# Kernel tuning notes

Hardware: AMD Instinct MI355X
Metric: run time of the kernel (lower is better)

## Reference

```python
import jax, jax.numpy as jnp
import numpy as np

K = 3
STRIDE = 1
PAD = 1
DIL = 1


def setup_inputs() -> dict:
    key = jax.random.key(0)
    k1, k2, k3, k4 = jax.random.split(key, 4)
    B, C, H, W = 8, 64, 96, 96
    O = 64
    x = jax.random.normal(k1, (B, C, H, W), jnp.float32)
    # offset-predicting conv is conventionally near-zero init -> small offsets
    w_off = jax.random.normal(k2, (2 * K * K, C, K, K), jnp.float32) * 0.01
    b_off = jax.random.normal(k3, (2 * K * K,), jnp.float32) * 0.01
    w_dcn = jax.random.normal(k4, (O, C, K, K), jnp.float32) * (1.0 / np.sqrt(C * K * K))
    return {"x": x, "w_off": w_off, "b_off": b_off, "w_dcn": w_dcn}


def _deform_conv(x, offset, w_dcn):
    B, C, H, W = x.shape
    O = w_dcn.shape[0]
    Ho, Wo = offset.shape[2], offset.shape[3]
    K2 = K * K
    # torchvision layout: offset[:, 2*k] = dy, offset[:, 2*k+1] = dx, k = ky*K + kx
    off = offset.reshape(B, K2, 2, Ho, Wo)
    kk = jnp.arange(K2)
    ky = (kk // K).astype(jnp.float32)
    kx = (kk % K).astype(jnp.float32)
    base_h = (jnp.arange(Ho) * STRIDE - PAD).astype(jnp.float32)
    base_w = (jnp.arange(Wo) * STRIDE - PAD).astype(jnp.float32)
    # sampling positions, shape [B, K2, Ho, Wo]
    py = off[:, :, 0] + base_h[None, None, :, None] + (ky * DIL)[None, :, None, None]
    px = off[:, :, 1] + base_w[None, None, None, :] + (kx * DIL)[None, :, None, None]

    y0 = jnp.floor(py)
    x0 = jnp.floor(px)
    wy = py - y0
    wx = px - x0
    y0i = y0.astype(jnp.int32)
    x0i = x0.astype(jnp.int32)
    y1i = y0i + 1
    x1i = x0i + 1

    x_flat = x.reshape(B, C, H * W)
    N = K2 * Ho * Wo

    def gather(yi, xi):
        valid = (yi >= 0) & (yi < H) & (xi >= 0) & (xi < W)
        lin = jnp.clip(yi, 0, H - 1) * W + jnp.clip(xi, 0, W - 1)  # [B,K2,Ho,Wo]
        idx = jnp.broadcast_to(lin.reshape(B, 1, N), (B, C, N))
        v = jnp.take_along_axis(x_flat, idx, axis=2).reshape(B, C, K2, Ho, Wo)
        return v * valid[:, None].astype(x.dtype)

    w00 = ((1 - wy) * (1 - wx))[:, None]
    w01 = ((1 - wy) * wx)[:, None]
    w10 = (wy * (1 - wx))[:, None]
    w11 = (wy * wx)[:, None]
    sampled = (gather(y0i, x0i) * w00 + gather(y0i, x1i) * w01
               + gather(y1i, x0i) * w10 + gather(y1i, x1i) * w11)  # [B,C,K2,Ho,Wo]

    # deformable conv = contraction over (c_in, kernel pos); bias=False
    return jnp.einsum('bckhw,ock->bohw', sampled, w_dcn.reshape(O, C, K2))


def reference(x, w_off, b_off, w_dcn):
    offset = jax.lax.conv_general_dilated(
        x, w_off, window_strides=(STRIDE, STRIDE), padding=[(PAD, PAD), (PAD, PAD)],
        rhs_dilation=(DIL, DIL), dimension_numbers=('NCHW', 'OIHW', 'NCHW'))
    offset = offset + b_off[None, :, None, None]
    return _deform_conv(x, offset, w_dcn)
```

## Files before the change

kernel.cpp:

```cpp
#include <hip/hip_runtime.h>

#define BB 8
#define CC 64
#define HH 96
#define WW 96
#define OO 64
#define KK 3
#define K2 9
#define HW (HH*WW)
#define NOFF 18
#define NPIX (BB*HW)
#define MT 64
#define NTILE (HW/MT)
#define NXCD 8
#define WR 6
#define WC 36
#define NWIN (WR*WC)
#define OSTR 21

typedef _Float16 f16;
typedef __attribute__((ext_vector_type(2))) _Float16 f16x2;
typedef __attribute__((ext_vector_type(4))) _Float16 f16x4;
typedef __attribute__((ext_vector_type(4))) float f32x4;
typedef __attribute__((ext_vector_type(2))) unsigned int uint2v;
typedef __attribute__((ext_vector_type(4))) unsigned int uint4v;

#define MFMA16(a,b,c) __builtin_amdgcn_mfma_f32_16x16x16f16(a,b,c,0,0,0)

__device__ __forceinline__ f16x2 bch(unsigned u) { return __builtin_bit_cast(f16x2, u); }
__device__ __forceinline__ unsigned bcu(f16x2 h) { return __builtin_bit_cast(unsigned, h); }
__device__ __forceinline__ f16x4 fq(unsigned a, unsigned b) {
  uint2v u = {a, b};
  return __builtin_bit_cast(f16x4, u);
}
__device__ __forceinline__ f16x4 fq2(uint2v u) { return __builtin_bit_cast(f16x4, u); }
__device__ __forceinline__ int xcd_remap(int bid, int per) {
  return (bid & 7) * per + (bid >> 3);
}

__global__ __launch_bounds__(256) void transpose_kernel(
    const float* __restrict__ x, unsigned short* __restrict__ xt) {
  int t = threadIdx.x;
  int px = xcd_remap(blockIdx.x, NPIX / 64 / NXCD) * 64 + (t & 63);
  int cg = t >> 6;
  int b = px / HW, hw = px % HW;
  const float* xp = x + (size_t)b * CC * HW + (size_t)(cg * 16) * HW + hw;
  f16 r[16];
  #pragma unroll
  for (int i = 0; i < 16; ++i) r[i] = (f16)xp[i * HW];
  uint4v v0, v1;
  #pragma unroll
  for (int q = 0; q < 4; ++q) {
    f16x2 a = {r[q*2], r[q*2+1]};       v0[q] = bcu(a);
    f16x2 bq = {r[8+q*2], r[8+q*2+1]};  v1[q] = bcu(bq);
  }
  uint4v* dst = (uint4v*)(xt + (size_t)px * CC + cg * 16);
  dst[0] = v0; dst[1] = v1;
}

__global__ void wprep_kernel(const float* __restrict__ w_dcn,
                             unsigned short* __restrict__ wtx) {
  int idx = blockIdx.x * 256 + threadIdx.x;
  int e = idx & 15;
  int l = (idx >> 4) & 63;
  int nb = (idx >> 10) & 3;
  int k = idx >> 12;
  int c = 16 * (l >> 4) + e;
  int o = nb * 16 + (l & 15);
  f16 h = (f16)w_dcn[(o * CC + c) * K2 + k];
  wtx[idx] = __builtin_bit_cast(unsigned short, h);
}

__global__ void woffprep_kernel(const float* __restrict__ w_off,
                                unsigned short* __restrict__ wofx) {
  int idx = blockIdx.x * 256 + threadIdx.x;
  int e = idx & 3;
  int l = (idx >> 2) & 63;
  int q = (idx >> 8) & 3;
  int n = (idx >> 10) & 1;
  int kt = idx >> 11;
  int c = q * 16 + 4 * (l >> 4) + e;
  int j = n * 16 + (l & 15);
  f16 h = (f16)((j < NOFF) ? w_off[(j * CC + c) * K2 + kt] : 0.f);
  wofx[idx] = __builtin_bit_cast(unsigned short, h);
}

#define XWIN_OFF 0
#define OFFS_OFF 27648
#define ACCX_OFF 0
#define SMEM_SZ  33024

__global__ __launch_bounds__(512, 4) void fused_kernel(
    const unsigned short* __restrict__ xt,
    const unsigned short* __restrict__ wofx,
    const float* __restrict__ b_off,
    const unsigned short* __restrict__ wtx,
    float* __restrict__ out) {
  __shared__ __align__(16) char smem[SMEM_SZ];
  char* xwin = smem + XWIN_OFF;
  float* offs = (float*)(smem + OFFS_OFF);
  float* accx = (float*)(smem + ACCX_OFF);

  int t = threadIdx.x;
  int blk = xcd_remap(blockIdx.x, NPIX / MT / NXCD);
  int b = blk / NTILE;
  int ti = blk % NTILE;
  int tr = ti / 3, tc = ti % 3;
  int h0 = tr * 2, w0 = tc * 32;
  int hw0 = h0 * WW + w0;

  const char* xb = (const char*)(xt + (size_t)b * HW * CC);

  #pragma unroll
  for (int r = 0; r < 4; ++r) {
    int d = r * 512 + t;
    if (d < NWIN * 8) {
      int row = d >> 3, sg = d & 7;
      int wr_ = row / WC, wc_ = row - wr_ * WC;
      int gy = h0 - 2 + wr_;
      int gx = w0 - 2 + wc_;
      uint4v v = (uint4v){0u, 0u, 0u, 0u};
      if (((unsigned)gy < HH) && ((unsigned)gx < WW))
        v = *(const uint4v*)(xb + (size_t)((gy * WW + gx) << 7) + (sg << 4));
      *(uint4v*)&xwin[row * 128 + ((sg ^ (row & 7)) << 4)] = v;
    }
  }
  __syncthreads();

  int wv = t >> 6;
  int l  = t & 63;
  int lr = l & 15, lh = l >> 4;

  {
    int m = wv & 3, n = wv >> 2;
    int p = m * 16 + lr;
    int prow = ((p >> 5) + 1) * WC + (p & 31) + 1;
    f32x4 accO = (f32x4){0.f, 0.f, 0.f, 0.f};
    #pragma unroll
    for (int kt = 0; kt < K2; ++kt) {
      int wrow = prow + (kt / 3) * WC + (kt % 3);
      int rs = wrow & 7;
      const char* bp = (const char*)wofx + (((size_t)(kt * 2 + n) * 4) * 64 + l) * 8;
      #pragma unroll
      for (int q = 0; q < 4; ++q) {
        uint2v a2 = *(const uint2v*)&xwin[wrow * 128
                      + ((((q << 1) + (lh >> 1)) ^ rs) << 4) + ((lh & 1) << 3)];
        uint2v b2 = *(const uint2v*)(bp + (size_t)q * (64 * 8));
        accO = MFMA16(fq2(a2), fq2(b2), accO);
      }
    }
    int j = n * 16 + lr;
    if (j < NOFF) {
      float bj = b_off[j];
      #pragma unroll
      for (int r = 0; r < 4; ++r) {
        int px = m * 16 + lh * 4 + r;
        offs[px * OSTR + j] = accO[r] + bj;
      }
    }
  }
  __syncthreads();

  int grp = wv >> 2;
  int base = grp * 5;
  int cnt  = 5 - grp;
  int Ra = (wv & 3) * 16 + lr;
  int hpix = h0 + (Ra >> 5), wpix = w0 + (Ra & 31);
  int cB = lh * 32;

  unsigned po01[5], po23[5], pw01[5], pw23[5];
  unsigned emask = 0;
  #pragma unroll
  for (int i = 0; i < 5; ++i) {
    po01[i] = 0; po23[i] = 0; pw01[i] = 0; pw23[i] = 0;
    if (i < cnt) {
      int kt = base + i;
      int ky = kt / 3, kx = kt % 3;
      float py = offs[Ra * OSTR + 2 * kt]     + (float)(hpix - 1 + ky);
      float px = offs[Ra * OSTR + 2 * kt + 1] + (float)(wpix - 1 + kx);
      float y0f = floorf(py), x0f = floorf(px);
      float wy = py - y0f, wx = px - x0f;
      int y0 = (int)y0f, x0 = (int)x0f;
      int y1 = y0 + 1, x1 = x0 + 1;
      bool vy0 = (unsigned)y0 < HH, vy1 = (unsigned)y1 < HH;
      bool vx0 = (unsigned)x0 < WW, vx1 = (unsigned)x1 < WW;
      int cy0 = min(max(y0, 0), HH - 1), cy1 = min(max(y1, 0), HH - 1);
      int cx0 = min(max(x0, 0), WW - 1), cx1 = min(max(x1, 0), WW - 1);
      float g00 = (1.f - wy) * (1.f - wx) * ((vy0 && vx0) ? 1.f : 0.f);
      float g01 = (1.f - wy) * wx         * ((vy0 && vx1) ? 1.f : 0.f);
      float g10 = wy * (1.f - wx)         * ((vy1 && vx0) ? 1.f : 0.f);
      float g11 = wy * wx                 * ((vy1 && vx1) ? 1.f : 0.f);
      int ry0 = cy0 - (h0 - 2), ry1 = cy1 - (h0 - 2);
      int rx0 = cx0 - (w0 - 2), rx1 = cx1 - (w0 - 2);
      bool inw = ((unsigned)ry0 < WR) && ((unsigned)ry1 < WR) &&
                 ((unsigned)rx0 < WC) && ((unsigned)rx1 < WC);
      if (inw) {
        po01[i] = (unsigned)((ry0 * WC + rx0) << 7)
                | ((unsigned)((ry0 * WC + rx1) << 7) << 16);
        po23[i] = (unsigned)((ry1 * WC + rx0) << 7)
                | ((unsigned)((ry1 * WC + rx1) << 7) << 16);
      } else {
        po01[i] = (unsigned)(cy0 * WW + cx0)
                | ((unsigned)(cy0 * WW + cx1) << 16) | 0x80000000u;
        po23[i] = (unsigned)(cy1 * WW + cx0)
                | ((unsigned)(cy1 * WW + cx1) << 16);
        emask |= 1u << i;
      }
      f16x2 wa = {(f16)g00, (f16)g01};
      f16x2 wb = {(f16)g10, (f16)g11};
      pw01[i] = bcu(wa);
      pw23[i] = bcu(wb);
    }
  }

  f32x4 acc[4];
  #pragma unroll
  for (int nb = 0; nb < 4; ++nb) acc[nb] = (f32x4){0.f, 0.f, 0.f, 0.f};

  #define WREAD(bo, pos) (*(const uint4v*)&xwin[(bo) + ((pos) << 4)])
  if (__ballot(emask != 0) == 0ull) {
    #pragma unroll
    for (int i = 0; i < 5; ++i) {
      if (i < cnt) {
        unsigned e0 = po01[i], e1 = po23[i];
        int i0 = (int)(e0 & 0xffffu), i1 = (int)(e0 >> 16);
        int i2 = (int)(e1 & 0xffffu), i3 = (int)(e1 >> 16);
        int s0 = lh * 2;
        uint4v c0a = WREAD(i0, s0 ^ ((i0 >> 7) & 7));
        uint4v c0b = WREAD(i0, (s0 + 1) ^ ((i0 >> 7) & 7));
        uint4v c1a = WREAD(i1, s0 ^ ((i1 >> 7) & 7));
        uint4v c1b = WREAD(i1, (s0 + 1) ^ ((i1 >> 7) & 7));
        uint4v c2a = WREAD(i2, s0 ^ ((i2 >> 7) & 7));
        uint4v c2b = WREAD(i2, (s0 + 1) ^ ((i2 >> 7) & 7));
        uint4v c3a = WREAD(i3, s0 ^ ((i3 >> 7) & 7));
        uint4v c3b = WREAD(i3, (s0 + 1) ^ ((i3 >> 7) & 7));
        f16x2 wA = bch(pw01[i]), wB = bch(pw23[i]);
        f16x2 p0 = {wA[0], wA[0]}, p1 = {wA[1], wA[1]};
        f16x2 p2 = {wB[0], wB[0]}, p3 = {wB[1], wB[1]};
        uint4v pa, pb2;
        #pragma unroll
        for (int q = 0; q < 4; ++q) {
          f16x2 s  = p0 * bch(c0a[q]) + p1 * bch(c1a[q])
                   + p2 * bch(c2a[q]) + p3 * bch(c3a[q]);
          pa[q] = bcu(s);
          f16x2 s2 = p0 * bch(c0b[q]) + p1 * bch(c1b[q])
                   + p2 * bch(c2b[q]) + p3 * bch(c3b[q]);
          pb2[q] = bcu(s2);
        }
        f16x4 a0 = fq(pa[0],  pa[1]);
        f16x4 a1 = fq(pa[2],  pa[3]);
        f16x4 a2 = fq(pb2[0], pb2[1]);
        f16x4 a3 = fq(pb2[2], pb2[3]);
        const char* wbase = (const char*)wtx
                          + (((size_t)(base + i) * 4) * 64 + l) * 32;
        #pragma unroll
        for (int nb = 0; nb < 4; ++nb) {
          const char* wp = wbase + (size_t)nb * (64 * 32);
          uint4v u0 = *(const uint4v*)wp;
          uint4v u1 = *(const uint4v*)(wp + 16);
          acc[nb] = MFMA16(a0, fq(u0[0], u0[1]), acc[nb]);
          acc[nb] = MFMA16(a1, fq(u0[2], u0[3]), acc[nb]);
          acc[nb] = MFMA16(a2, fq(u1[0], u1[1]), acc[nb]);
          acc[nb] = MFMA16(a3, fq(u1[2], u1[3]), acc[nb]);
        }
      }
    }
  } else {
    #pragma unroll
    for (int i = 0; i < 5; ++i) {
      if (i < cnt) {
        unsigned e0 = po01[i], e1 = po23[i];
        uint4v c0a, c0b, c1a, c1b, c2a, c2b, c3a, c3b;
        if ((int)e0 >= 0) {
          int i0 = (int)(e0 & 0xffffu), i1 = (int)(e0 >> 16);
          int i2 = (int)(e1 & 0xffffu), i3 = (int)(e1 >> 16);
          int s0 = lh * 2;
          c0a = WREAD(i0, s0 ^ ((i0 >> 7) & 7));
          c0b = WREAD(i0, (s0 + 1) ^ ((i0 >> 7) & 7));
          c1a = WREAD(i1, s0 ^ ((i1 >> 7) & 7));
          c1b = WREAD(i1, (s0 + 1) ^ ((i1 >> 7) & 7));
          c2a = WREAD(i2, s0 ^ ((i2 >> 7) & 7));
          c2b = WREAD(i2, (s0 + 1) ^ ((i2 >> 7) & 7));
          c3a = WREAD(i3, s0 ^ ((i3 >> 7) & 7));
          c3b = WREAD(i3, (s0 + 1) ^ ((i3 >> 7) & 7));
        } else {
          int i0 = (int)(e0 & 0x7fffu) << 7;
          int i1 = (int)((e0 >> 16) & 0x7fffu) << 7;
          int i2 = (int)(e1 & 0x7fffu) << 7;
          int i3 = (int)((e1 >> 16) & 0x7fffu) << 7;
          c0a = *(const uint4v*)(xb + i0 + cB);
          c0b = *(const uint4v*)(xb + i0 + cB + 16);
          c1a = *(const uint4v*)(xb + i1 + cB);
          c1b = *(const uint4v*)(xb + i1 + cB + 16);
          c2a = *(const uint4v*)(xb + i2 + cB);
          c2b = *(const uint4v*)(xb + i2 + cB + 16);
          c3a = *(const uint4v*)(xb + i3 + cB);
          c3b = *(const uint4v*)(xb + i3 + cB + 16);
        }
        f16x2 wA = bch(pw01[i]), wB = bch(pw23[i]);
        f16x2 p0 = {wA[0], wA[0]}, p1 = {wA[1], wA[1]};
        f16x2 p2 = {wB[0], wB[0]}, p3 = {wB[1], wB[1]};
        uint4v pa, pb2;
        #pragma unroll
        for (int q = 0; q < 4; ++q) {
          f16x2 s  = p0 * bch(c0a[q]) + p1 * bch(c1a[q])
                   + p2 * bch(c2a[q]) + p3 * bch(c3a[q]);
          pa[q] = bcu(s);
          f16x2 s2 = p0 * bch(c0b[q]) + p1 * bch(c1b[q])
                   + p2 * bch(c2b[q]) + p3 * bch(c3b[q]);
          pb2[q] = bcu(s2);
        }
        f16x4 a0 = fq(pa[0],  pa[1]);
        f16x4 a1 = fq(pa[2],  pa[3]);
        f16x4 a2 = fq(pb2[0], pb2[1]);
        f16x4 a3 = fq(pb2[2], pb2[3]);
        const char* wbase = (const char*)wtx
                          + (((size_t)(base + i) * 4) * 64 + l) * 32;
        #pragma unroll
        for (int nb = 0; nb < 4; ++nb) {
          const char* wp = wbase + (size_t)nb * (64 * 32);
          uint4v u0 = *(const uint4v*)wp;
          uint4v u1 = *(const uint4v*)(wp + 16);
          acc[nb] = MFMA16(a0, fq(u0[0], u0[1]), acc[nb]);
          acc[nb] = MFMA16(a1, fq(u0[2], u0[3]), acc[nb]);
          acc[nb] = MFMA16(a2, fq(u1[0], u1[1]), acc[nb]);
          acc[nb] = MFMA16(a3, fq(u1[2], u1[3]), acc[nb]);
        }
      }
    }
  }
  __syncthreads();

  if (grp == 1) {
    #pragma unroll
    for (int nb = 0; nb < 4; ++nb)
      *(f32x4*)&accx[(nb * 16 + lr) * 68 + (wv & 3) * 16 + lh * 4] = acc[nb];
  }
  __syncthreads();
  if (grp == 0) {
    float* ob = out + (size_t)b * OO * HW;
    #pragma unroll
    for (int nb = 0; nb < 4; ++nb) {
      f32x4 other = *(const f32x4*)&accx[(nb * 16 + lr) * 68 + (wv & 3) * 16 + lh * 4];
      f32x4 v = acc[nb] + other;
      int o = nb * 16 + lr;
      int m = (wv & 3) * 16 + lh * 4;
      int base2 = hw0 + (m >> 5) * WW + (m & 31);
      *(f32x4*)(ob + (size_t)o * HW + base2) = v;
    }
  }
}

extern "C" void kernel_launch(void* const* d_in, const int* in_sizes, int n_in,
                              void* d_out, int out_size, void* d_ws, size_t ws_size,
                              hipStream_t stream) {
  const float* x     = (const float*)d_in[0];
  const float* w_off = (const float*)d_in[1];
  const float* b_off = (const float*)d_in[2];
  const float* w_dcn = (const float*)d_in[3];
  float* out = (float*)d_out;

  char* ws = (char*)d_ws;
  unsigned short* xtp  = (unsigned short*)ws;
  unsigned short* wtx  = (unsigned short*)(ws + 9437184);
  unsigned short* wofx = (unsigned short*)(ws + 9437184 + 73728);

  transpose_kernel<<<NPIX / 64, 256, 0, stream>>>(x, xtp);
  wprep_kernel<<<(K2 * 4 * 64 * 16) / 256, 256, 0, stream>>>(w_dcn, wtx);
  woffprep_kernel<<<(K2 * 2 * 4 * 64 * 4) / 256, 256, 0, stream>>>(w_off, wofx);
  fused_kernel<<<NPIX / MT, 512, 0, stream>>>(xtp, wofx, b_off, wtx, out);
}
```

Before: 47.04 us.

## Double pixel tile per block, drop split-K reduction, merge weight prep kernels

```diff
diff --git a/kernel.cpp b/kernel.cpp
--- a/kernel.cpp
+++ b/kernel.cpp
@@ -10,10 +10,10 @@
 #define HW (HH*WW)
 #define NOFF 18
 #define NPIX (BB*HW)
-#define MT 64
+#define MT 128
 #define NTILE (HW/MT)
 #define NXCD 8
-#define WR 6
+#define WR 8
 #define WC 36
 #define NWIN (WR*WC)
 #define OSTR 21
@@ -58,39 +58,39 @@
   dst[0] = v0; dst[1] = v1;
 }
 
-__global__ void wprep_kernel(const float* __restrict__ w_dcn,
-                             unsigned short* __restrict__ wtx) {
+__global__ void prep_kernel(const float* __restrict__ w_dcn,
+                            const float* __restrict__ w_off,
+                            unsigned short* __restrict__ wtx,
+                            unsigned short* __restrict__ wofx) {
   int idx = blockIdx.x * 256 + threadIdx.x;
-  int e = idx & 15;
-  int l = (idx >> 4) & 63;
-  int nb = (idx >> 10) & 3;
-  int k = idx >> 12;
-  int c = 16 * (l >> 4) + e;
-  int o = nb * 16 + (l & 15);
-  f16 h = (f16)w_dcn[(o * CC + c) * K2 + k];
-  wtx[idx] = __builtin_bit_cast(unsigned short, h);
-}
-
-__global__ void woffprep_kernel(const float* __restrict__ w_off,
-                                unsigned short* __restrict__ wofx) {
-  int idx = blockIdx.x * 256 + threadIdx.x;
-  int e = idx & 3;
-  int l = (idx >> 2) & 63;
-  int q = (idx >> 8) & 3;
-  int n = (idx >> 10) & 1;
-  int kt = idx >> 11;
-  int c = q * 16 + 4 * (l >> 4) + e;
-  int j = n * 16 + (l & 15);
-  f16 h = (f16)((j < NOFF) ? w_off[(j * CC + c) * K2 + kt] : 0.f);
-  wofx[idx] = __builtin_bit_cast(unsigned short, h);
+  if (idx < 36864) {
+    int e = idx & 15;
+    int l = (idx >> 4) & 63;
+    int nb = (idx >> 10) & 3;
+    int k = idx >> 12;
+    int c = 16 * (l >> 4) + e;
+    int o = nb * 16 + (l & 15);
+    f16 h = (f16)w_dcn[(o * CC + c) * K2 + k];
+    wtx[idx] = __builtin_bit_cast(unsigned short, h);
+  } else {
+    int i2 = idx - 36864;
+    int e = i2 & 3;
+    int l = (i2 >> 2) & 63;
+    int q = (i2 >> 8) & 3;
+    int n = (i2 >> 10) & 1;
+    int kt = i2 >> 11;
+    int c = q * 16 + 4 * (l >> 4) + e;
+    int j = n * 16 + (l & 15);
+    f16 h = (f16)((j < NOFF) ? w_off[(j * CC + c) * K2 + kt] : 0.f);
+    wofx[i2] = __builtin_bit_cast(unsigned short, h);
+  }
 }
 
 #define XWIN_OFF 0
-#define OFFS_OFF 27648
-#define ACCX_OFF 0
-#define SMEM_SZ  33024
-
-__global__ __launch_bounds__(512, 4) void fused_kernel(
+#define OFFS_OFF 36864
+#define SMEM_SZ  47616
+
+__global__ __launch_bounds__(512, 3) void fused_kernel(
     const unsigned short* __restrict__ xt,
     const unsigned short* __restrict__ wofx,
     const float* __restrict__ b_off,
@@ -99,20 +99,19 @@
   __shared__ __align__(16) char smem[SMEM_SZ];
   char* xwin = smem + XWIN_OFF;
   float* offs = (float*)(smem + OFFS_OFF);
-  float* accx = (float*)(smem + ACCX_OFF);
 
   int t = threadIdx.x;
   int blk = xcd_remap(blockIdx.x, NPIX / MT / NXCD);
   int b = blk / NTILE;
   int ti = blk % NTILE;
   int tr = ti / 3, tc = ti % 3;
-  int h0 = tr * 2, w0 = tc * 32;
+  int h0 = tr * 4, w0 = tc * 32;
   int hw0 = h0 * WW + w0;
 
   const char* xb = (const char*)(xt + (size_t)b * HW * CC);
 
   #pragma unroll
-  for (int r = 0; r < 4; ++r) {
+  for (int r = 0; r < 5; ++r) {
     int d = r * 512 + t;
     if (d < NWIN * 8) {
       int row = d >> 3, sg = d & 7;
@@ -132,222 +131,210 @@
   int lr = l & 15, lh = l >> 4;
 
   {
-    int m = wv & 3, n = wv >> 2;
-    int p = m * 16 + lr;
+    int p = wv * 16 + lr;
     int prow = ((p >> 5) + 1) * WC + (p & 31) + 1;
-    f32x4 accO = (f32x4){0.f, 0.f, 0.f, 0.f};
+    f32x4 accO0 = (f32x4){0.f, 0.f, 0.f, 0.f};
+    f32x4 accO1 = (f32x4){0.f, 0.f, 0.f, 0.f};
     #pragma unroll
     for (int kt = 0; kt < K2; ++kt) {
       int wrow = prow + (kt / 3) * WC + (kt % 3);
       int rs = wrow & 7;
-      const char* bp = (const char*)wofx + (((size_t)(kt * 2 + n) * 4) * 64 + l) * 8;
+      const char* bp0 = (const char*)wofx + (((size_t)(kt * 2 + 0) * 4) * 64 + l) * 8;
+      const char* bp1 = (const char*)wofx + (((size_t)(kt * 2 + 1) * 4) * 64 + l) * 8;
       #pragma unroll
       for (int q = 0; q < 4; ++q) {
         uint2v a2 = *(const uint2v*)&xwin[wrow * 128
                       + ((((q << 1) + (lh >> 1)) ^ rs) << 4) + ((lh & 1) << 3)];
-        uint2v b2 = *(const uint2v*)(bp + (size_t)q * (64 * 8));
-        accO = MFMA16(fq2(a2), fq2(b2), accO);
-      }
-    }
-    int j = n * 16 + lr;
-    if (j < NOFF) {
+        uint2v b0 = *(const uint2v*)(bp0 + (size_t)q * (64 * 8));
+        uint2v b1 = *(const uint2v*)(bp1 + (size_t)q * (64 * 8));
+        accO0 = MFMA16(fq2(a2), fq2(b0), accO0);
+        accO1 = MFMA16(fq2(a2), fq2(b1), accO1);
+      }
+    }
+    {
+      int j = lr;
       float bj = b_off[j];
       #pragma unroll
       for (int r = 0; r < 4; ++r) {
-        int px = m * 16 + lh * 4 + r;
-        offs[px * OSTR + j] = accO[r] + bj;
+        int px = wv * 16 + lh * 4 + r;
+        offs[px * OSTR + j] = accO0[r] + bj;
+      }
+    }
+    if (lr < 2) {
+      int j = 16 + lr;
+      float bj = b_off[j];
+      #pragma unroll
+      for (int r = 0; r < 4; ++r) {
+        int px = wv * 16 + lh * 4 + r;
+        offs[px * OSTR + j] = accO1[r] + bj;
       }
     }
   }
   __syncthreads();
 
-  int grp = wv >> 2;
-  int base = grp * 5;
-  int cnt  = 5 - grp;
-  int Ra = (wv & 3) * 16 + lr;
+  int Ra = wv * 16 + lr;
   int hpix = h0 + (Ra >> 5), wpix = w0 + (Ra & 31);
   int cB = lh * 32;
 
-  unsigned po01[5], po23[5], pw01[5], pw23[5];
+  unsigned po01[K2], po23[K2], pw01[K2], pw23[K2];
   unsigned emask = 0;
   #pragma unroll
-  for (int i = 0; i < 5; ++i) {
-    po01[i] = 0; po23[i] = 0; pw01[i] = 0; pw23[i] = 0;
-    if (i < cnt) {
-      int kt = base + i;
-      int ky = kt / 3, kx = kt % 3;
-      float py = offs[Ra * OSTR + 2 * kt]     + (float)(hpix - 1 + ky);
-      float px = offs[Ra * OSTR + 2 * kt + 1] + (float)(wpix - 1 + kx);
-      float y0f = floorf(py), x0f = floorf(px);
-      float wy = py - y0f, wx = px - x0f;
-      int y0 = (int)y0f, x0 = (int)x0f;
-      int y1 = y0 + 1, x1 = x0 + 1;
-      bool vy0 = (unsigned)y0 < HH, vy1 = (unsigned)y1 < HH;
-      bool vx0 = (unsigned)x0 < WW, vx1 = (unsigned)x1 < WW;
-      int cy0 = min(max(y0, 0), HH - 1), cy1 = min(max(y1, 0), HH - 1);
-      int cx0 = min(max(x0, 0), WW - 1), cx1 = min(max(x1, 0), WW - 1);
-      float g00 = (1.f - wy) * (1.f - wx) * ((vy0 && vx0) ? 1.f : 0.f);
-      float g01 = (1.f - wy) * wx         * ((vy0 && vx1) ? 1.f : 0.f);
-      float g10 = wy * (1.f - wx)         * ((vy1 && vx0) ? 1.f : 0.f);
-      float g11 = wy * wx                 * ((vy1 && vx1) ? 1.f : 0.f);
-      int ry0 = cy0 - (h0 - 2), ry1 = cy1 - (h0 - 2);
-      int rx0 = cx0 - (w0 - 2), rx1 = cx1 - (w0 - 2);
-      bool inw = ((unsigned)ry0 < WR) && ((unsigned)ry1 < WR) &&
-                 ((unsigned)rx0 < WC) && ((unsigned)rx1 < WC);
-      if (inw) {
-        po01[i] = (unsigned)((ry0 * WC + rx0) << 7)
-                | ((unsigned)((ry0 * WC + rx1) << 7) << 16);
-        po23[i] = (unsigned)((ry1 * WC + rx0) << 7)
-                | ((unsigned)((ry1 * WC + rx1) << 7) << 16);
-      } else {
-        po01[i] = (unsigned)(cy0 * WW + cx0)
-                | ((unsigned)(cy0 * WW + cx1) << 16) | 0x80000000u;
-        po23[i] = (unsigned)(cy1 * WW + cx0)
-                | ((unsigned)(cy1 * WW + cx1) << 16);
-        emask |= 1u << i;
-      }
-      f16x2 wa = {(f16)g00, (f16)g01};
-      f16x2 wb = {(f16)g10, (f16)g11};
-      pw01[i] = bcu(wa);
-      pw23[i] = bcu(wb);
-    }
+  for (int k = 0; k < K2; ++k) {
+    int ky = k / KK, kx = k % KK;
+    float py = offs[Ra * OSTR + 2 * k]     + (float)(hpix - 1 + ky);
+    float px = offs[Ra * OSTR + 2 * k + 1] + (float)(wpix - 1 + kx);
+    float y0f = floorf(py), x0f = floorf(px);
+    float wy = py - y0f, wx = px - x0f;
+    int y0 = (int)y0f, x0 = (int)x0f;
+    int y1 = y0 + 1, x1 = x0 + 1;
+    bool vy0 = (unsigned)y0 < HH, vy1 = (unsigned)y1 < HH;
+    bool vx0 = (unsigned)x0 < WW, vx1 = (unsigned)x1 < WW;
+    int cy0 = min(max(y0, 0), HH - 1), cy1 = min(max(y1, 0), HH - 1);
+    int cx0 = min(max(x0, 0), WW - 1), cx1 = min(max(x1, 0), WW - 1);
+    float g00 = (1.f - wy) * (1.f - wx) * ((vy0 && vx0) ? 1.f : 0.f);
+    float g01 = (1.f - wy) * wx         * ((vy0 && vx1) ? 1.f : 0.f);
+    float g10 = wy * (1.f - wx)         * ((vy1 && vx0) ? 1.f : 0.f);
+    float g11 = wy * wx                 * ((vy1 && vx1) ? 1.f : 0.f);
+    int ry0 = cy0 - (h0 - 2), ry1 = cy1 - (h0 - 2);
+    int rx0 = cx0 - (w0 - 2), rx1 = cx1 - (w0 - 2);
+    bool inw = ((unsigned)ry0 < WR) && ((unsigned)ry1 < WR) &&
+               ((unsigned)rx0 < WC) && ((unsigned)rx1 < WC);
+    if (inw) {
+      po01[k] = (unsigned)(ry0 * WC + rx0)
+              | ((unsigned)(ry0 * WC + rx1) << 16);
+      po23[k] = (unsigned)(ry1 * WC + rx0)
+              | ((unsigned)(ry1 * WC + rx1) << 16);
+    } else {
+      po01[k] = (unsigned)(cy0 * WW + cx0)
+              | ((unsigned)(cy0 * WW + cx1) << 16) | 0x80000000u;
+      po23[k] = (unsigned)(cy1 * WW + cx0)
+              | ((unsigned)(cy1 * WW + cx1) << 16);
+      emask |= 1u << k;
+    }
+    f16x2 wa = {(f16)g00, (f16)g01};
+    f16x2 wb = {(f16)g10, (f16)g11};
+    pw01[k] = bcu(wa);
+    pw23[k] = bcu(wb);
   }
 
   f32x4 acc[4];
   #pragma unroll
   for (int nb = 0; nb < 4; ++nb) acc[nb] = (f32x4){0.f, 0.f, 0.f, 0.f};
 
-  #define WREAD(bo, pos) (*(const uint4v*)&xwin[(bo) + ((pos) << 4)])
+  #define WREAD(ro, pos) (*(const uint4v*)&xwin[((ro) << 7) + ((pos) << 4)])
   if (__ballot(emask != 0) == 0ull) {
     #pragma unroll
-    for (int i = 0; i < 5; ++i) {
-      if (i < cnt) {
-        unsigned e0 = po01[i], e1 = po23[i];
-        int i0 = (int)(e0 & 0xffffu), i1 = (int)(e0 >> 16);
-        int i2 = (int)(e1 & 0xffffu), i3 = (int)(e1 >> 16);
-        int s0 = lh * 2;
-        uint4v c0a = WREAD(i0, s0 ^ ((i0 >> 7) & 7));
-        uint4v c0b = WREAD(i0, (s0 + 1) ^ ((i0 >> 7) & 7));
-        uint4v c1a = WREAD(i1, s0 ^ ((i1 >> 7) & 7));
-        uint4v c1b = WREAD(i1, (s0 + 1) ^ ((i1 >> 7) & 7));
-        uint4v c2a = WREAD(i2, s0 ^ ((i2 >> 7) & 7));
-        uint4v c2b = WREAD(i2, (s0 + 1) ^ ((i2 >> 7) & 7));
-        uint4v c3a = WREAD(i3, s0 ^ ((i3 >> 7) & 7));
-        uint4v c3b = WREAD(i3, (s0 + 1) ^ ((i3 >> 7) & 7));
-        f16x2 wA = bch(pw01[i]), wB = bch(pw23[i]);
-        f16x2 p0 = {wA[0], wA[0]}, p1 = {wA[1], wA[1]};
-        f16x2 p2 = {wB[0], wB[0]}, p3 = {wB[1], wB[1]};
-        uint4v pa, pb2;
-        #pragma unroll
-        for (int q = 0; q < 4; ++q) {
-          f16x2 s  = p0 * bch(c0a[q]) + p1 * bch(c1a[q])
-                   + p2 * bch(c2a[q]) + p3 * bch(c3a[q]);
-          pa[q] = bcu(s);
-          f16x2 s2 = p0 * bch(c0b[q]) + p1 * bch(c1b[q])
-                   + p2 * bch(c2b[q]) + p3 * bch(c3b[q]);
-          pb2[q] = bcu(s2);
-        }
-        f16x4 a0 = fq(pa[0],  pa[1]);
-        f16x4 a1 = fq(pa[2],  pa[3]);
-        f16x4 a2 = fq(pb2[0], pb2[1]);
-        f16x4 a3 = fq(pb2[2], pb2[3]);
-        const char* wbase = (const char*)wtx
-                          + (((size_t)(base + i) * 4) * 64 + l) * 32;
-        #pragma unroll
-        for (int nb = 0; nb < 4; ++nb) {
-          const char* wp = wbase + (size_t)nb * (64 * 32);
-          uint4v u0 = *(const uint4v*)wp;
-          uint4v u1 = *(const uint4v*)(wp + 16);
-          acc[nb] = MFMA16(a0, fq(u0[0], u0[1]), acc[nb]);
-          acc[nb] = MFMA16(a1, fq(u0[2], u0[3]), acc[nb]);
-          acc[nb] = MFMA16(a2, fq(u1[0], u1[1]), acc[nb]);
-          acc[nb] = MFMA16(a3, fq(u1[2], u1[3]), acc[nb]);
-        }
+    for (int k = 0; k < K2; ++k) {
+      unsigned e0 = po01[k], e1 = po23[k];
+      int r0 = (int)(e0 & 0x7fffu), r1 = (int)(e0 >> 16);
+      int r2 = (int)(e1 & 0x7fffu), r3 = (int)(e1 >> 16);
+      int s0 = lh * 2;
+      uint4v c0a = WREAD(r0, s0 ^ (r0 & 7));
+      uint4v c0b = WREAD(r0, (s0 + 1) ^ (r0 & 7));
+      uint4v c1a = WREAD(r1, s0 ^ (r1 & 7));
+      uint4v c1b = WREAD(r1, (s0 + 1) ^ (r1 & 7));
+      uint4v c2a = WREAD(r2, s0 ^ (r2 & 7));
+      uint4v c2b = WREAD(r2, (s0 + 1) ^ (r2 & 7));
+      uint4v c3a = WREAD(r3, s0 ^ (r3 & 7));
+      uint4v c3b = WREAD(r3, (s0 + 1) ^ (r3 & 7));
+      f16x2 wA = bch(pw01[k]), wB = bch(pw23[k]);
+      f16x2 p0 = {wA[0], wA[0]}, p1 = {wA[1], wA[1]};
+      f16x2 p2 = {wB[0], wB[0]}, p3 = {wB[1], wB[1]};
+      uint4v pa, pb2;
+      #pragma unroll
+      for (int q = 0; q < 4; ++q) {
+        f16x2 s  = p0 * bch(c0a[q]) + p1 * bch(c1a[q])
+                 + p2 * bch(c2a[q]) + p3 * bch(c3a[q]);
+        pa[q] = bcu(s);
+        f16x2 s2 = p0 * bch(c0b[q]) + p1 * bch(c1b[q])
+                 + p2 * bch(c2b[q]) + p3 * bch(c3b[q]);
+        pb2[q] = bcu(s2);
+      }
+      f16x4 a0 = fq(pa[0],  pa[1]);
+      f16x4 a1 = fq(pa[2],  pa[3]);
+      f16x4 a2 = fq(pb2[0], pb2[1]);
+      f16x4 a3 = fq(pb2[2], pb2[3]);
+      const char* wbase = (const char*)wtx + (((size_t)k * 4) * 64 + l) * 32;
+      #pragma unroll
+      for (int nb = 0; nb < 4; ++nb) {
+        const char* wp = wbase + (size_t)nb * (64 * 32);
+        uint4v u0 = *(const uint4v*)wp;
+        uint4v u1 = *(const uint4v*)(wp + 16);
+        acc[nb] = MFMA16(a0, fq(u0[0], u0[1]), acc[nb]);
+        acc[nb] = MFMA16(a1, fq(u0[2], u0[3]), acc[nb]);
+        acc[nb] = MFMA16(a2, fq(u1[0], u1[1]), acc[nb]);
+        acc[nb] = MFMA16(a3, fq(u1[2], u1[3]), acc[nb]);
       }
     }
   } else {
     #pragma unroll
-    for (int i = 0; i < 5; ++i) {
-      if (i < cnt) {
-        unsigned e0 = po01[i], e1 = po23[i];
-        uint4v c0a, c0b, c1a, c1b, c2a, c2b, c3a, c3b;
-        if ((int)e0 >= 0) {
-          int i0 = (int)(e0 & 0xffffu), i1 = (int)(e0 >> 16);
-          int i2 = (int)(e1 & 0xffffu), i3 = (int)(e1 >> 16);
-          int s0 = lh * 2;
-          c0a = WREAD(i0, s0 ^ ((i0 >> 7) & 7));
-          c0b = WREAD(i0, (s0 + 1) ^ ((i0 >> 7) & 7));
-          c1a = WREAD(i1, s0 ^ ((i1 >> 7) & 7));
-          c1b = WREAD(i1, (s0 + 1) ^ ((i1 >> 7) & 7));
-          c2a = WREAD(i2, s0 ^ ((i2 >> 7) & 7));
-          c2b = WREAD(i2, (s0 + 1) ^ ((i2 >> 7) & 7));
-          c3a = WREAD(i3, s0 ^ ((i3 >> 7) & 7));
-          c3b = WREAD(i3, (s0 + 1) ^ ((i3 >> 7) & 7));
-        } else {
-          int i0 = (int)(e0 & 0x7fffu) << 7;
-          int i1 = (int)((e0 >> 16) & 0x7fffu) << 7;
-          int i2 = (int)(e1 & 0x7fffu) << 7;
-          int i3 = (int)((e1 >> 16) & 0x7fffu) << 7;
-          c0a = *(const uint4v*)(xb + i0 + cB);
-          c0b = *(const uint4v*)(xb + i0 + cB + 16);
-          c1a = *(const uint4v*)(xb + i1 + cB);
-          c1b = *(const uint4v*)(xb + i1 + cB + 16);
-          c2a = *(const uint4v*)(xb + i2 + cB);
-          c2b = *(const uint4v*)(xb + i2 + cB + 16);
-          c3a = *(const uint4v*)(xb + i3 + cB);
-          c3b = *(const uint4v*)(xb + i3 + cB + 16);
-        }
-        f16x2 wA = bch(pw01[i]), wB = bch(pw23[i]);
-        f16x2 p0 = {wA[0], wA[0]}, p1 = {wA[1], wA[1]};
-        f16x2 p2 = {wB[0], wB[0]}, p3 = {wB[1], wB[1]};
-        uint4v pa, pb2;
-        #pragma unroll
-        for (int q = 0; q < 4; ++q) {
-          f16x2 s  = p0 * bch(c0a[q]) + p1 * bch(c1a[q])
-                   + p2 * bch(c2a[q]) + p3 * bch(c3a[q]);
-          pa[q] = bcu(s);
-          f16x2 s2 = p0 * bch(c0b[q]) + p1 * bch(c1b[q])
-                   + p2 * bch(c2b[q]) + p3 * bch(c3b[q]);
-          pb2[q] = bcu(s2);
-        }
-        f16x4 a0 = fq(pa[0],  pa[1]);
-        f16x4 a1 = fq(pa[2],  pa[3]);
-        f16x4 a2 = fq(pb2[0], pb2[1]);
-        f16x4 a3 = fq(pb2[2], pb2[3]);
-        const char* wbase = (const char*)wtx
-                          + (((size_t)(base + i) * 4) * 64 + l) * 32;
-        #pragma unroll
-        for (int nb = 0; nb < 4; ++nb) {
-          const char* wp = wbase + (size_t)nb * (64 * 32);
-          uint4v u0 = *(const uint4v*)wp;
-          uint4v u1 = *(const uint4v*)(wp + 16);
-          acc[nb] = MFMA16(a0, fq(u0[0], u0[1]), acc[nb]);
-          acc[nb] = MFMA16(a1, fq(u0[2], u0[3]), acc[nb]);
-          acc[nb] = MFMA16(a2, fq(u1[0], u1[1]), acc[nb]);
-          acc[nb] = MFMA16(a3, fq(u1[2], u1[3]), acc[nb]);
-        }
-      }
-    }
-  }
-  __syncthreads();
-
-  if (grp == 1) {
-    #pragma unroll
-    for (int nb = 0; nb < 4; ++nb)
-      *(f32x4*)&accx[(nb * 16 + lr) * 68 + (wv & 3) * 16 + lh * 4] = acc[nb];
-  }
-  __syncthreads();
-  if (grp == 0) {
-    float* ob = out + (size_t)b * OO * HW;
-    #pragma unroll
-    for (int nb = 0; nb < 4; ++nb) {
-      f32x4 other = *(const f32x4*)&accx[(nb * 16 + lr) * 68 + (wv & 3) * 16 + lh * 4];
-      f32x4 v = acc[nb] + other;
-      int o = nb * 16 + lr;
-      int m = (wv & 3) * 16 + lh * 4;
-      int base2 = hw0 + (m >> 5) * WW + (m & 31);
-      *(f32x4*)(ob + (size_t)o * HW + base2) = v;
-    }
+    for (int k = 0; k < K2; ++k) {
+      unsigned e0 = po01[k], e1 = po23[k];
+      uint4v c0a, c0b, c1a, c1b, c2a, c2b, c3a, c3b;
+      if ((int)e0 >= 0) {
+        int r0 = (int)(e0 & 0x7fffu), r1 = (int)(e0 >> 16);
+        int r2 = (int)(e1 & 0x7fffu), r3 = (int)(e1 >> 16);
+        int s0 = lh * 2;
+        c0a = WREAD(r0, s0 ^ (r0 & 7));
+        c0b = WREAD(r0, (s0 + 1) ^ (r0 & 7));
+        c1a = WREAD(r1, s0 ^ (r1 & 7));
+        c1b = WREAD(r1, (s0 + 1) ^ (r1 & 7));
+        c2a = WREAD(r2, s0 ^ (r2 & 7));
+        c2b = WREAD(r2, (s0 + 1) ^ (r2 & 7));
+        c3a = WREAD(r3, s0 ^ (r3 & 7));
+        c3b = WREAD(r3, (s0 + 1) ^ (r3 & 7));
+      } else {
+        int i0 = (int)(e0 & 0x7fffu) << 7;
+        int i1 = (int)((e0 >> 16) & 0x7fffu) << 7;
+        int i2 = (int)(e1 & 0x7fffu) << 7;
+        int i3 = (int)((e1 >> 16) & 0x7fffu) << 7;
+        c0a = *(const uint4v*)(xb + i0 + cB);
+        c0b = *(const uint4v*)(xb + i0 + cB + 16);
+        c1a = *(const uint4v*)(xb + i1 + cB);
+        c1b = *(const uint4v*)(xb + i1 + cB + 16);
+        c2a = *(const uint4v*)(xb + i2 + cB);
+        c2b = *(const uint4v*)(xb + i2 + cB + 16);
+        c3a = *(const uint4v*)(xb + i3 + cB);
+        c3b = *(const uint4v*)(xb + i3 + cB + 16);
+      }
+      f16x2 wA = bch(pw01[k]), wB = bch(pw23[k]);
+      f16x2 p0 = {wA[0], wA[0]}, p1 = {wA[1], wA[1]};
+      f16x2 p2 = {wB[0], wB[0]}, p3 = {wB[1], wB[1]};
+      uint4v pa, pb2;
+      #pragma unroll
+      for (int q = 0; q < 4; ++q) {
+        f16x2 s  = p0 * bch(c0a[q]) + p1 * bch(c1a[q])
+                 + p2 * bch(c2a[q]) + p3 * bch(c3a[q]);
+        pa[q] = bcu(s);
+        f16x2 s2 = p0 * bch(c0b[q]) + p1 * bch(c1b[q])
+                 + p2 * bch(c2b[q]) + p3 * bch(c3b[q]);
+        pb2[q] = bcu(s2);
+      }
+      f16x4 a0 = fq(pa[0],  pa[1]);
+      f16x4 a1 = fq(pa[2],  pa[3]);
+      f16x4 a2 = fq(pb2[0], pb2[1]);
+      f16x4 a3 = fq(pb2[2], pb2[3]);
+      const char* wbase = (const char*)wtx + (((size_t)k * 4) * 64 + l) * 32;
+      #pragma unroll
+      for (int nb = 0; nb < 4; ++nb) {
+        const char* wp = wbase + (size_t)nb * (64 * 32);
+        uint4v u0 = *(const uint4v*)wp;
+        uint4v u1 = *(const uint4v*)(wp + 16);
+        acc[nb] = MFMA16(a0, fq(u0[0], u0[1]), acc[nb]);
+        acc[nb] = MFMA16(a1, fq(u0[2], u0[3]), acc[nb]);
+        acc[nb] = MFMA16(a2, fq(u1[0], u1[1]), acc[nb]);
+        acc[nb] = MFMA16(a3, fq(u1[2], u1[3]), acc[nb]);
+      }
+    }
+  }
+
+  float* ob = out + (size_t)b * OO * HW;
+  #pragma unroll
+  for (int nb = 0; nb < 4; ++nb) {
+    int o = nb * 16 + lr;
+    int m = wv * 16 + lh * 4;
+    int base2 = hw0 + (m >> 5) * WW + (m & 31);
+    *(f32x4*)(ob + (size_t)o * HW + base2) = acc[nb];
   }
 }
 
@@ -366,7 +353,6 @@
   unsigned short* wofx = (unsigned short*)(ws + 9437184 + 73728);
 
   transpose_kernel<<<NPIX / 64, 256, 0, stream>>>(x, xtp);
-  wprep_kernel<<<(K2 * 4 * 64 * 16) / 256, 256, 0, stream>>>(w_dcn, wtx);
-  woffprep_kernel<<<(K2 * 2 * 4 * 64 * 4) / 256, 256, 0, stream>>>(w_off, wofx);
+  prep_kernel<<<(36864 + 18432) / 256, 256, 0, stream>>>(w_dcn, w_off, wtx, wofx);
   fused_kernel<<<NPIX / MT, 512, 0, stream>>>(xtp, wofx, b_off, wtx, out);
 }
```

After: 60.64 us. +28.9%, slower.
